# Kernel tuning notes

Measured on AMD Instinct MI355X. Metric: run time of the kernel, lower is better.

The kernel has to match this reference:

```python
import jax, jax.numpy as jnp
import numpy as np

NUM_USERS = 100000
NUM_ITEMS = 50000
D = 64            # args.recdim
N_LAYERS = 3      # args.layer
NNZ = 4800000     # edges in the normalized bipartite adjacency (COO)
N = NUM_USERS + NUM_ITEMS


def setup_inputs() -> dict:
    key = jax.random.key(0)
    k1, k2, k3, k4, k5 = jax.random.split(key, 5)
    # LightGCN inits embeddings with normal(std=0.1)
    user_emb = 0.1 * jax.random.normal(k1, (NUM_USERS, D), dtype=jnp.float32)
    item_emb = 0.1 * jax.random.normal(k2, (NUM_ITEMS, D), dtype=jnp.float32)
    adj_rows = jax.random.randint(k3, (NNZ,), 0, N)
    adj_cols = jax.random.randint(k4, (NNZ,), 0, N)
    # stand-in for D^{-1/2} A D^{-1/2} normalized values
    adj_vals = jax.random.uniform(k5, (NNZ,), dtype=jnp.float32)
    return {"user_emb": user_emb, "item_emb": item_emb,
            "adj_vals": adj_vals, "adj_rows": adj_rows, "adj_cols": adj_cols}


def _spmm(rows, cols, vals, x, n):
    # sparse [n,n] @ dense [n,d] via gather + segment-sum (COO SpMM)
    return jax.ops.segment_sum(vals[:, None] * x[cols], rows, num_segments=n)


def reference(user_emb, item_emb, adj_vals, adj_rows, adj_cols):
    n_users = user_emb.shape[0]
    n = n_users + item_emb.shape[0]
    all_emb = jnp.concatenate([user_emb, item_emb], axis=0)  # [N, D]
    embs = [all_emb]
    for _ in range(N_LAYERS):  # fixed small hop count
        all_emb = _spmm(adj_rows, adj_cols, adj_vals, all_emb, n)
        embs.append(all_emb)
    light_out = jnp.mean(jnp.stack(embs, axis=1), axis=1)  # [N, D]
    users = light_out[:n_users]
    items = light_out[n_users:]
    return users, items
```

## Files before the change

kernel.cpp:

```cpp
#include <hip/hip_runtime.h>


#define NUSERS 100000
#define NITEMS 50000
#define NTOT   150000
#define DIM    64
#define NNZ_E  4800000

#define RPB     256
#define RSH     8
#define NBUCK   586
#define CHUNK_E 8192
#define NPART   ((NNZ_E + CHUNK_E - 1) / CHUNK_E)
#define NCB     37
#define CSH     12
#define NBIN    (RPB * NCB)

__device__ __forceinline__ unsigned short benc(float f) {
    union { float f; unsigned u; } t; t.f = f;
    unsigned r = t.u + 0x7FFFu + ((t.u >> 16) & 1u);
    return (unsigned short)(r >> 16);
}
__device__ __forceinline__ float blo(unsigned g) { return __uint_as_float(g << 16); }
__device__ __forceinline__ float bhi(unsigned g) { return __uint_as_float(g & 0xFFFF0000u); }

__global__ void __launch_bounds__(512)
partA2_kernel(const int* __restrict__ rows, const int* __restrict__ cols,
              const float* __restrict__ vals, int* __restrict__ cntmat,
              int* __restrict__ segoff, int2* __restrict__ tmp) {
    __shared__ int2 buf[CHUNK_E];
    __shared__ int cnt[NBUCK];
    __shared__ int st[512];
    int p = blockIdx.x;
    int c0 = p * CHUNK_E;
    int c1 = c0 + CHUNK_E; if (c1 > NNZ_E) c1 = NNZ_E;
    int nb = c1 - c0;
    int tid = threadIdx.x;
    for (int k = tid; k < NBUCK; k += 512) cnt[k] = 0;
    __syncthreads();
    int rloc[16];
#pragma unroll
    for (int u = 0; u < 16; ++u) {
        int e = c0 + tid + u * 512;
        rloc[u] = (e < c1) ? rows[e] : -1;
        if (rloc[u] >= 0) atomicAdd(&cnt[rloc[u] >> RSH], 1);
    }
    __syncthreads();
    int t0 = tid * 2;
    int cA = (t0     < NBUCK) ? cnt[t0]     : 0;
    int cB = (t0 + 1 < NBUCK) ? cnt[t0 + 1] : 0;
    int s = cA + cB;
    st[tid] = s;
    __syncthreads();
    for (int ofs = 1; ofs < 512; ofs <<= 1) {
        int a = (tid >= ofs) ? st[tid - ofs] : 0;
        __syncthreads();
        st[tid] += a;
        __syncthreads();
    }
    int P = st[tid] - s;
    if (t0 < NBUCK) {
        cnt[t0] = P;
        segoff[(size_t)p * NBUCK + t0] = P;
        cntmat[(size_t)p * NBUCK + t0] = cA;
    }
    if (t0 + 1 < NBUCK) {
        cnt[t0 + 1] = P + cA;
        segoff[(size_t)p * NBUCK + t0 + 1] = P + cA;
        cntmat[(size_t)p * NBUCK + t0 + 1] = cB;
    }
    __syncthreads();
#pragma unroll
    for (int u = 0; u < 16; ++u) {
        int e = c0 + tid + u * 512;
        if (rloc[u] >= 0) {
            int r = rloc[u];
            int b = r >> RSH, rl = r & (RPB - 1);
            int q = atomicAdd(&cnt[b], 1);
            buf[q] = make_int2(cols[e] | (rl << 18), __float_as_int(vals[e]));
        }
    }
    __syncthreads();
    for (int k = tid; k < nb; k += 512)
        tmp[c0 + k] = buf[k];
}

__global__ void __launch_bounds__(1024)
colscan1_kernel(const int* __restrict__ cntmat, int* __restrict__ runoffT,
                int* __restrict__ colTotal) {
    __shared__ int t[1024];
    int b = blockIdx.x;
    int tid = threadIdx.x;
    int v = (tid < NPART) ? cntmat[(size_t)tid * NBUCK + b] : 0;
    t[tid] = v;
    __syncthreads();
    for (int ofs = 1; ofs < 1024; ofs <<= 1) {
        int a = (tid >= ofs) ? t[tid - ofs] : 0;
        __syncthreads();
        t[tid] += a;
        __syncthreads();
    }
    if (tid < NPART) runoffT[(size_t)b * (NPART + 1) + tid] = t[tid] - v;
    if (tid == NPART - 1) {
        runoffT[(size_t)b * (NPART + 1) + NPART] = t[tid];
        colTotal[b] = t[tid];
    }
}

__global__ void __launch_bounds__(1024)
colscan2_kernel(const int* __restrict__ colTotal, int* __restrict__ bptr) {
    __shared__ int t[1024];
    int tid = threadIdx.x;
    int v = (tid < NBUCK) ? colTotal[tid] : 0;
    t[tid] = v;
    __syncthreads();
    for (int ofs = 1; ofs < 1024; ofs <<= 1) {
        int a = (tid >= ofs) ? t[tid - ofs] : 0;
        __syncthreads();
        t[tid] += a;
        __syncthreads();
    }
    if (tid < NBUCK) bptr[tid] = t[tid] - v;
    if (tid == 1023) bptr[NBUCK] = t[1023];
}

__global__ void __launch_bounds__(1024)
partBF_kernel(const int* __restrict__ bptr, const int* __restrict__ runoffT,
              const int* __restrict__ segoff, const int2* __restrict__ tmp,
              unsigned* __restrict__ fin, int* __restrict__ rowptr) {
    __shared__ int cnt[NBIN];
    __shared__ int st[1024];
    __shared__ int runoff[NPART + 1];
    __shared__ int soff[NPART];
    int b = blockIdx.x;
    int bb0 = bptr[b];
    int tid = threadIdx.x;
    for (int k = tid; k < NBIN; k += 1024) cnt[k] = 0;
    if (tid <= NPART) runoff[tid] = runoffT[(size_t)b * (NPART + 1) + tid];
    if (tid < NPART)  soff[tid]   = segoff[(size_t)tid * NBUCK + b];
    __syncthreads();
    int nb = runoff[NPART];
    for (int j = tid; j < nb; j += 1024) {
        int lo = 0, hi = NPART;
        while (hi - lo > 1) { int mid = (lo + hi) >> 1; if (runoff[mid] <= j) lo = mid; else hi = mid; }
        int src = lo * CHUNK_E + soff[lo] + (j - runoff[lo]);
        int x = tmp[src].x;
        int key = ((x >> 18) & 255) * NCB + ((x & 0x3FFFF) >> CSH);
        atomicAdd(&cnt[key], 1);
    }
    __syncthreads();
    int t0 = tid * 10;
    int c[10];
    int s = 0;
#pragma unroll
    for (int u = 0; u < 10; ++u) {
        int idx = t0 + u;
        c[u] = (idx < NBIN) ? cnt[idx] : 0;
        s += c[u];
    }
    st[tid] = s;
    __syncthreads();
    for (int ofs = 1; ofs < 1024; ofs <<= 1) {
        int a = (tid >= ofs) ? st[tid - ofs] : 0;
        __syncthreads();
        st[tid] += a;
        __syncthreads();
    }
    int P = st[tid] - s;
#pragma unroll
    for (int u = 0; u < 10; ++u) {
        int idx = t0 + u;
        if (idx < NBIN) { cnt[idx] = P; P += c[u]; }
    }
    __syncthreads();
    if (tid < RPB) {
        int r = b * RPB + tid;
        if (r < NTOT) rowptr[r] = bb0 + cnt[tid * NCB];
    }
    if (b == NBUCK - 1 && tid == 0) rowptr[NTOT] = bb0 + nb;
    __syncthreads();
    for (int j = tid; j < nb; j += 1024) {
        int lo = 0, hi = NPART;
        while (hi - lo > 1) { int mid = (lo + hi) >> 1; if (runoff[mid] <= j) lo = mid; else hi = mid; }
        int src = lo * CHUNK_E + soff[lo] + (j - runoff[lo]);
        int2 t = tmp[src];
        int x = t.x;
        int key = ((x >> 18) & 255) * NCB + ((x & 0x3FFFF) >> CSH);
        int q = atomicAdd(&cnt[key], 1);
        unsigned qq = (unsigned)__float2int_rn(__int_as_float(t.y) * 4096.f);
        if (qq > 4095u) qq = 4095u;
        fin[bb0 + q] = ((unsigned)x & 0x3FFFFu) | (qq << 20);
    }
}

__global__ void convert_kernel(const float2* __restrict__ user, const float2* __restrict__ item,
                               unsigned* __restrict__ xh2) {
    int i = blockIdx.x * blockDim.x + threadIdx.x;
    if (i >= NTOT * 32) return;
    float2 v = (i < NUSERS * 32) ? user[i] : item[i - NUSERS * 32];
    xh2[i] = (unsigned)benc(v.x) | ((unsigned)benc(v.y) << 16);
}

__global__ void __launch_bounds__(256)
spmm_kernel(const int* __restrict__ rowptr, const unsigned* __restrict__ ed,
            const uint4* __restrict__ xin, uint4* __restrict__ yout,
            const float4* __restrict__ user, const float4* __restrict__ item,
            const uint4* __restrict__ y1, float4* __restrict__ out, int last) {
    int wid = blockIdx.x * (blockDim.x >> 6) + (threadIdx.x >> 6);
    int lane = threadIdx.x & 63;
    int oct = lane >> 3, s = lane & 7;
    int r = wid * 8 + oct;
    if (r >= NTOT) return;
    int start = rowptr[r];
    int end   = rowptr[r + 1];
    const float SCL = 1.f / 4096.f;
    float a0 = 0.f, a1 = 0.f, a2 = 0.f, a3 = 0.f, a4 = 0.f, a5 = 0.f, a6 = 0.f, a7 = 0.f;
    int i = start;
    for (; i + 8 <= end; i += 8) {
        unsigned e[8];
#pragma unroll
        for (int u = 0; u < 8; ++u) e[u] = ed[i + u];
        uint4 g[8];
#pragma unroll
        for (int u = 0; u < 8; ++u) g[u] = xin[(size_t)(e[u] & 0x3FFFFu) * 8 + s];
#pragma unroll
        for (int u = 0; u < 8; ++u) {
            float v = (float)(e[u] >> 20) * SCL;
            a0 += v * blo(g[u].x); a1 += v * bhi(g[u].x);
            a2 += v * blo(g[u].y); a3 += v * bhi(g[u].y);
            a4 += v * blo(g[u].z); a5 += v * bhi(g[u].z);
            a6 += v * blo(g[u].w); a7 += v * bhi(g[u].w);
        }
    }
    for (; i < end; ++i) {
        unsigned e = ed[i];
        uint4 g = xin[(size_t)(e & 0x3FFFFu) * 8 + s];
        float v = (float)(e >> 20) * SCL;
        a0 += v * blo(g.x); a1 += v * bhi(g.x);
        a2 += v * blo(g.y); a3 += v * bhi(g.y);
        a4 += v * blo(g.z); a5 += v * bhi(g.z);
        a6 += v * blo(g.w); a7 += v * bhi(g.w);
    }
    if (!last) {
        uint4 o;
        o.x = (unsigned)benc(a0) | ((unsigned)benc(a1) << 16);
        o.y = (unsigned)benc(a2) | ((unsigned)benc(a3) << 16);
        o.z = (unsigned)benc(a4) | ((unsigned)benc(a5) << 16);
        o.w = (unsigned)benc(a6) | ((unsigned)benc(a7) << 16);
        yout[(size_t)r * 8 + s] = o;
    } else {
        size_t f4 = (size_t)r * 16 + 2 * s;
        float4 x0a = (r < NUSERS) ? user[f4]     : item[f4     - (size_t)NUSERS * 16];
        float4 x0b = (r < NUSERS) ? user[f4 + 1] : item[f4 + 1 - (size_t)NUSERS * 16];
        uint4 u1 = y1[(size_t)r * 8 + s];
        uint4 u2 = xin[(size_t)r * 8 + s];
        float4 oa, ob;
        oa.x = 0.25f * (x0a.x + blo(u1.x) + blo(u2.x) + a0);
        oa.y = 0.25f * (x0a.y + bhi(u1.x) + bhi(u2.x) + a1);
        oa.z = 0.25f * (x0a.z + blo(u1.y) + blo(u2.y) + a2);
        oa.w = 0.25f * (x0a.w + bhi(u1.y) + bhi(u2.y) + a3);
        ob.x = 0.25f * (x0b.x + blo(u1.z) + blo(u2.z) + a4);
        ob.y = 0.25f * (x0b.y + bhi(u1.z) + bhi(u2.z) + a5);
        ob.z = 0.25f * (x0b.z + blo(u1.w) + blo(u2.w) + a6);
        ob.w = 0.25f * (x0b.w + bhi(u1.w) + bhi(u2.w) + a7);
        out[f4]     = oa;
        out[f4 + 1] = ob;
    }
}

extern "C" void kernel_launch(void* const* d_in, const int* in_sizes, int n_in,
                              void* d_out, int out_size, void* d_ws, size_t ws_size,
                              hipStream_t stream) {
    const float* user = (const float*)d_in[0];
    const float* item = (const float*)d_in[1];
    const float* vals = (const float*)d_in[2];
    const int*   rows = (const int*)d_in[3];
    const int*   cols = (const int*)d_in[4];
    float* out = (float*)d_out;

    char* w = (char*)d_ws;
    int2*     tmp      = (int2*)w;     w += (size_t)NNZ_E * 8;
    unsigned* fin      = (unsigned*)w; w += (size_t)NNZ_E * 4;
    unsigned* bufA     = (unsigned*)w; w += (size_t)NTOT * DIM * 2;
    unsigned* bufB     = (unsigned*)w; w += (size_t)NTOT * DIM * 2;
    int*      cntmat   = (int*)w;      w += (size_t)NPART * NBUCK * 4;
    int*      runoffT  = (int*)w;      w += (size_t)NBUCK * (NPART + 1) * 4;
    int*      segoff   = (int*)w;      w += (size_t)NPART * NBUCK * 4;
    int*      rowptr   = (int*)w;      w += (size_t)(NTOT + 1) * 4;
    int*      colTotal = (int*)w;      w += (size_t)NBUCK * 4;
    int*      bptr     = (int*)w;

    const int blk = 256;
    const int gConv = (NTOT * 32 + blk - 1) / blk;
    const int gSpmm = (NTOT / 8 + 3) / 4;

    partA2_kernel<<<NPART, 512, 0, stream>>>(rows, cols, vals, cntmat, segoff, tmp);
    colscan1_kernel<<<NBUCK, 1024, 0, stream>>>(cntmat, runoffT, colTotal);
    colscan2_kernel<<<1, 1024, 0, stream>>>(colTotal, bptr);
    partBF_kernel<<<NBUCK, 1024, 0, stream>>>(bptr, runoffT, segoff, tmp, fin, rowptr);

    convert_kernel<<<gConv, blk, 0, stream>>>((const float2*)user, (const float2*)item, bufA);

    spmm_kernel<<<gSpmm, blk, 0, stream>>>(rowptr, fin, (const uint4*)bufA, (uint4*)bufB,
                                           (const float4*)user, (const float4*)item,
                                           (const uint4*)bufB, (float4*)out, 0);
    spmm_kernel<<<gSpmm, blk, 0, stream>>>(rowptr, fin, (const uint4*)bufB, (uint4*)bufA,
                                           (const float4*)user, (const float4*)item,
                                           (const uint4*)bufB, (float4*)out, 0);
    spmm_kernel<<<gSpmm, blk, 0, stream>>>(rowptr, fin, (const uint4*)bufA, (uint4*)bufA,
                                           (const float4*)user, (const float4*)item,
                                           (const uint4*)bufB, (float4*)out, 1);
}
```

Baseline: 489.3 us.

## Interleave edges of four rows into padded quad groups for vectorized SpMM

```diff
diff --git a/kernel.cpp b/kernel.cpp
--- a/kernel.cpp
+++ b/kernel.cpp
@@ -15,6 +15,8 @@
 #define NCB     37
 #define CSH     12
 #define NBIN    (RPB * NCB)
+#define NOCT    (NBUCK * 64)
+#define FINCAP  6400000
 
 __device__ __forceinline__ unsigned short benc(float f) {
     union { float f; unsigned u; } t; t.f = f;
@@ -86,8 +88,7 @@
 }
 
 __global__ void __launch_bounds__(1024)
-colscan1_kernel(const int* __restrict__ cntmat, int* __restrict__ runoffT,
-                int* __restrict__ colTotal) {
+colscan1_kernel(const int* __restrict__ cntmat, int* __restrict__ runoffT) {
     __shared__ int t[1024];
     int b = blockIdx.x;
     int tid = threadIdx.x;
@@ -101,43 +102,69 @@
         __syncthreads();
     }
     if (tid < NPART) runoffT[(size_t)b * (NPART + 1) + tid] = t[tid] - v;
-    if (tid == NPART - 1) {
-        runoffT[(size_t)b * (NPART + 1) + NPART] = t[tid];
-        colTotal[b] = t[tid];
-    }
+    if (tid == NPART - 1) runoffT[(size_t)b * (NPART + 1) + NPART] = t[tid];
+}
+
+__global__ void __launch_bounds__(256)
+degcnt_kernel(const int* __restrict__ rows, int* __restrict__ deg) {
+    int i = blockIdx.x * 256 + threadIdx.x;
+    int stride = gridDim.x * 256;
+    for (; i < NNZ_E; i += stride) atomicAdd(&deg[rows[i]], 1);
+}
+
+__global__ void __launch_bounds__(256)
+ogmax_kernel(const int* __restrict__ deg, int* __restrict__ p4) {
+    int og = blockIdx.x * 256 + threadIdx.x;
+    if (og >= NOCT) return;
+    int4 d = ((const int4*)deg)[og];
+    int m = max(max(d.x, d.y), max(d.z, d.w));
+    p4[og] = 4 * m;
 }
 
 __global__ void __launch_bounds__(1024)
-colscan2_kernel(const int* __restrict__ colTotal, int* __restrict__ bptr) {
-    __shared__ int t[1024];
+ogscan_kernel(const int* __restrict__ p4, int* __restrict__ ogptr) {
+    __shared__ int st[1024];
     int tid = threadIdx.x;
-    int v = (tid < NBUCK) ? colTotal[tid] : 0;
-    t[tid] = v;
+    int base = tid * 37;
+    int sum = 0;
+#pragma unroll 4
+    for (int u = 0; u < 37; ++u) {
+        int og = base + u;
+        if (og < NOCT) sum += p4[og];
+    }
+    st[tid] = sum;
     __syncthreads();
     for (int ofs = 1; ofs < 1024; ofs <<= 1) {
-        int a = (tid >= ofs) ? t[tid - ofs] : 0;
-        __syncthreads();
-        t[tid] += a;
-        __syncthreads();
-    }
-    if (tid < NBUCK) bptr[tid] = t[tid] - v;
-    if (tid == 1023) bptr[NBUCK] = t[1023];
+        int a = (tid >= ofs) ? st[tid - ofs] : 0;
+        __syncthreads();
+        st[tid] += a;
+        __syncthreads();
+    }
+    int P = st[tid] - sum;
+#pragma unroll 4
+    for (int u = 0; u < 37; ++u) {
+        int og = base + u;
+        if (og < NOCT) { ogptr[og] = P; P += p4[og]; }
+    }
+    if (tid == 1023) ogptr[NOCT] = st[1023];
 }
 
 __global__ void __launch_bounds__(1024)
-partBF_kernel(const int* __restrict__ bptr, const int* __restrict__ runoffT,
-              const int* __restrict__ segoff, const int2* __restrict__ tmp,
-              unsigned* __restrict__ fin, int* __restrict__ rowptr) {
+partBF_kernel(const int* __restrict__ runoffT, const int* __restrict__ segoff,
+              const int2* __restrict__ tmp, const int* __restrict__ ogptr,
+              unsigned* __restrict__ fin) {
     __shared__ int cnt[NBIN];
     __shared__ int st[1024];
     __shared__ int runoff[NPART + 1];
     __shared__ int soff[NPART];
+    __shared__ int rowbase[RPB];
+    __shared__ int ogbase[64];
     int b = blockIdx.x;
-    int bb0 = bptr[b];
     int tid = threadIdx.x;
     for (int k = tid; k < NBIN; k += 1024) cnt[k] = 0;
     if (tid <= NPART) runoff[tid] = runoffT[(size_t)b * (NPART + 1) + tid];
     if (tid < NPART)  soff[tid]   = segoff[(size_t)tid * NBUCK + b];
+    if (tid < 64)     ogbase[tid] = ogptr[b * 64 + tid];
     __syncthreads();
     int nb = runoff[NPART];
     for (int j = tid; j < nb; j += 1024) {
@@ -173,11 +200,7 @@
         if (idx < NBIN) { cnt[idx] = P; P += c[u]; }
     }
     __syncthreads();
-    if (tid < RPB) {
-        int r = b * RPB + tid;
-        if (r < NTOT) rowptr[r] = bb0 + cnt[tid * NCB];
-    }
-    if (b == NBUCK - 1 && tid == 0) rowptr[NTOT] = bb0 + nb;
+    if (tid < RPB) rowbase[tid] = cnt[tid * NCB];
     __syncthreads();
     for (int j = tid; j < nb; j += 1024) {
         int lo = 0, hi = NPART;
@@ -185,11 +208,14 @@
         int src = lo * CHUNK_E + soff[lo] + (j - runoff[lo]);
         int2 t = tmp[src];
         int x = t.x;
-        int key = ((x >> 18) & 255) * NCB + ((x & 0x3FFFF) >> CSH);
+        int rl = (x >> 18) & 255;
+        int key = rl * NCB + ((x & 0x3FFFF) >> CSH);
         int q = atomicAdd(&cnt[key], 1);
+        int i = q - rowbase[rl];
+        int dest = ogbase[rl >> 2] + i * 4 + (rl & 3);
         unsigned qq = (unsigned)__float2int_rn(__int_as_float(t.y) * 4096.f);
         if (qq > 4095u) qq = 4095u;
-        fin[bb0 + q] = ((unsigned)x & 0x3FFFFu) | (qq << 20);
+        fin[dest] = ((unsigned)x & 0x3FFFFu) | (qq << 20);
     }
 }
 
@@ -201,70 +227,97 @@
     xh2[i] = (unsigned)benc(v.x) | ((unsigned)benc(v.y) << 16);
 }
 
-__global__ void __launch_bounds__(256)
-spmm_kernel(const int* __restrict__ rowptr, const unsigned* __restrict__ ed,
-            const uint4* __restrict__ xin, uint4* __restrict__ yout,
-            const float4* __restrict__ user, const float4* __restrict__ item,
-            const uint4* __restrict__ y1, float4* __restrict__ out, int last) {
-    int wid = blockIdx.x * (blockDim.x >> 6) + (threadIdx.x >> 6);
+__global__ void __launch_bounds__(256, 5)
+spmm5_kernel(const int* __restrict__ ogptr, const unsigned* __restrict__ ed,
+             const uint4* __restrict__ xin, uint4* __restrict__ yout,
+             const float4* __restrict__ user, const float4* __restrict__ item,
+             const uint4* __restrict__ y1, float4* __restrict__ out, int last) {
+    int wid  = blockIdx.x * 4 + (threadIdx.x >> 6);
     int lane = threadIdx.x & 63;
-    int oct = lane >> 3, s = lane & 7;
-    int r = wid * 8 + oct;
-    if (r >= NTOT) return;
-    int start = rowptr[r];
-    int end   = rowptr[r + 1];
+    int g    = wid * 8 + (lane >> 3);
+    int s    = lane & 7;
+    int i0   = ogptr[g];
+    int nt   = (ogptr[g + 1] - i0) >> 2;
+    const uint4* eq = (const uint4*)(ed + i0);
     const float SCL = 1.f / 4096.f;
-    float a0 = 0.f, a1 = 0.f, a2 = 0.f, a3 = 0.f, a4 = 0.f, a5 = 0.f, a6 = 0.f, a7 = 0.f;
-    int i = start;
-    for (; i + 8 <= end; i += 8) {
-        unsigned e[8];
-#pragma unroll
-        for (int u = 0; u < 8; ++u) e[u] = ed[i + u];
-        uint4 g[8];
-#pragma unroll
-        for (int u = 0; u < 8; ++u) g[u] = xin[(size_t)(e[u] & 0x3FFFFu) * 8 + s];
-#pragma unroll
-        for (int u = 0; u < 8; ++u) {
-            float v = (float)(e[u] >> 20) * SCL;
-            a0 += v * blo(g[u].x); a1 += v * bhi(g[u].x);
-            a2 += v * blo(g[u].y); a3 += v * bhi(g[u].y);
-            a4 += v * blo(g[u].z); a5 += v * bhi(g[u].z);
-            a6 += v * blo(g[u].w); a7 += v * bhi(g[u].w);
-        }
-    }
-    for (; i < end; ++i) {
-        unsigned e = ed[i];
-        uint4 g = xin[(size_t)(e & 0x3FFFFu) * 8 + s];
-        float v = (float)(e >> 20) * SCL;
-        a0 += v * blo(g.x); a1 += v * bhi(g.x);
-        a2 += v * blo(g.y); a3 += v * bhi(g.y);
-        a4 += v * blo(g.z); a5 += v * bhi(g.z);
-        a6 += v * blo(g.w); a7 += v * bhi(g.w);
-    }
+    float4 A00 = {0,0,0,0}, A01 = {0,0,0,0};
+    float4 A10 = {0,0,0,0}, A11 = {0,0,0,0};
+    float4 A20 = {0,0,0,0}, A21 = {0,0,0,0};
+    float4 A30 = {0,0,0,0}, A31 = {0,0,0,0};
+
+#define ACC(AK0, AK1, E, G) do { \
+        float v = (float)((E) >> 20) * SCL; \
+        AK0.x += v * blo((G).x); AK0.y += v * bhi((G).x); \
+        AK0.z += v * blo((G).y); AK0.w += v * bhi((G).y); \
+        AK1.x += v * blo((G).z); AK1.y += v * bhi((G).z); \
+        AK1.z += v * blo((G).w); AK1.w += v * bhi((G).w); \
+    } while (0)
+
+    int ii = 0;
+    for (; ii + 2 <= nt; ii += 2) {
+        uint4 Ea = eq[ii], Eb = eq[ii + 1];
+        uint4 G0 = xin[(size_t)(Ea.x & 0x3FFFFu) * 8 + s];
+        uint4 G1 = xin[(size_t)(Ea.y & 0x3FFFFu) * 8 + s];
+        uint4 G2 = xin[(size_t)(Ea.z & 0x3FFFFu) * 8 + s];
+        uint4 G3 = xin[(size_t)(Ea.w & 0x3FFFFu) * 8 + s];
+        uint4 G4 = xin[(size_t)(Eb.x & 0x3FFFFu) * 8 + s];
+        uint4 G5 = xin[(size_t)(Eb.y & 0x3FFFFu) * 8 + s];
+        uint4 G6 = xin[(size_t)(Eb.z & 0x3FFFFu) * 8 + s];
+        uint4 G7 = xin[(size_t)(Eb.w & 0x3FFFFu) * 8 + s];
+        ACC(A00, A01, Ea.x, G0); ACC(A10, A11, Ea.y, G1);
+        ACC(A20, A21, Ea.z, G2); ACC(A30, A31, Ea.w, G3);
+        ACC(A00, A01, Eb.x, G4); ACC(A10, A11, Eb.y, G5);
+        ACC(A20, A21, Eb.z, G6); ACC(A30, A31, Eb.w, G7);
+    }
+    if (ii < nt) {
+        uint4 Ea = eq[ii];
+        uint4 G0 = xin[(size_t)(Ea.x & 0x3FFFFu) * 8 + s];
+        uint4 G1 = xin[(size_t)(Ea.y & 0x3FFFFu) * 8 + s];
+        uint4 G2 = xin[(size_t)(Ea.z & 0x3FFFFu) * 8 + s];
+        uint4 G3 = xin[(size_t)(Ea.w & 0x3FFFFu) * 8 + s];
+        ACC(A00, A01, Ea.x, G0); ACC(A10, A11, Ea.y, G1);
+        ACC(A20, A21, Ea.z, G2); ACC(A30, A31, Ea.w, G3);
+    }
+#undef ACC
+
     if (!last) {
-        uint4 o;
-        o.x = (unsigned)benc(a0) | ((unsigned)benc(a1) << 16);
-        o.y = (unsigned)benc(a2) | ((unsigned)benc(a3) << 16);
-        o.z = (unsigned)benc(a4) | ((unsigned)benc(a5) << 16);
-        o.w = (unsigned)benc(a6) | ((unsigned)benc(a7) << 16);
-        yout[(size_t)r * 8 + s] = o;
+#define EPI(K, AK0, AK1) do { \
+        int r = g * 4 + (K); \
+        if (r < NTOT) { \
+            uint4 o; \
+            o.x = (unsigned)benc(AK0.x) | ((unsigned)benc(AK0.y) << 16); \
+            o.y = (unsigned)benc(AK0.z) | ((unsigned)benc(AK0.w) << 16); \
+            o.z = (unsigned)benc(AK1.x) | ((unsigned)benc(AK1.y) << 16); \
+            o.w = (unsigned)benc(AK1.z) | ((unsigned)benc(AK1.w) << 16); \
+            yout[(size_t)r * 8 + s] = o; \
+        } \
+    } while (0)
+        EPI(0, A00, A01); EPI(1, A10, A11); EPI(2, A20, A21); EPI(3, A30, A31);
+#undef EPI
     } else {
-        size_t f4 = (size_t)r * 16 + 2 * s;
-        float4 x0a = (r < NUSERS) ? user[f4]     : item[f4     - (size_t)NUSERS * 16];
-        float4 x0b = (r < NUSERS) ? user[f4 + 1] : item[f4 + 1 - (size_t)NUSERS * 16];
-        uint4 u1 = y1[(size_t)r * 8 + s];
-        uint4 u2 = xin[(size_t)r * 8 + s];
-        float4 oa, ob;
-        oa.x = 0.25f * (x0a.x + blo(u1.x) + blo(u2.x) + a0);
-        oa.y = 0.25f * (x0a.y + bhi(u1.x) + bhi(u2.x) + a1);
-        oa.z = 0.25f * (x0a.z + blo(u1.y) + blo(u2.y) + a2);
-        oa.w = 0.25f * (x0a.w + bhi(u1.y) + bhi(u2.y) + a3);
-        ob.x = 0.25f * (x0b.x + blo(u1.z) + blo(u2.z) + a4);
-        ob.y = 0.25f * (x0b.y + bhi(u1.z) + bhi(u2.z) + a5);
-        ob.z = 0.25f * (x0b.z + blo(u1.w) + blo(u2.w) + a6);
-        ob.w = 0.25f * (x0b.w + bhi(u1.w) + bhi(u2.w) + a7);
-        out[f4]     = oa;
-        out[f4 + 1] = ob;
+#define EPI(K, AK0, AK1) do { \
+        int r = g * 4 + (K); \
+        if (r < NTOT) { \
+            size_t f4 = (size_t)r * 16 + 2 * s; \
+            float4 x0a = (r < NUSERS) ? user[f4]     : item[f4     - (size_t)NUSERS * 16]; \
+            float4 x0b = (r < NUSERS) ? user[f4 + 1] : item[f4 + 1 - (size_t)NUSERS * 16]; \
+            uint4 u1 = y1[(size_t)r * 8 + s]; \
+            uint4 u2 = xin[(size_t)r * 8 + s]; \
+            float4 oa, ob; \
+            oa.x = 0.25f * (x0a.x + blo(u1.x) + blo(u2.x) + AK0.x); \
+            oa.y = 0.25f * (x0a.y + bhi(u1.x) + bhi(u2.x) + AK0.y); \
+            oa.z = 0.25f * (x0a.z + blo(u1.y) + blo(u2.y) + AK0.z); \
+            oa.w = 0.25f * (x0a.w + bhi(u1.y) + bhi(u2.y) + AK0.w); \
+            ob.x = 0.25f * (x0b.x + blo(u1.z) + blo(u2.z) + AK1.x); \
+            ob.y = 0.25f * (x0b.y + bhi(u1.z) + bhi(u2.z) + AK1.y); \
+            ob.z = 0.25f * (x0b.z + blo(u1.w) + blo(u2.w) + AK1.z); \
+            ob.w = 0.25f * (x0b.w + bhi(u1.w) + bhi(u2.w) + AK1.w); \
+            out[f4]     = oa; \
+            out[f4 + 1] = ob; \
+        } \
+    } while (0)
+        EPI(0, A00, A01); EPI(1, A10, A11); EPI(2, A20, A21); EPI(3, A30, A31);
+#undef EPI
     }
 }
 
@@ -279,35 +332,41 @@
     float* out = (float*)d_out;
 
     char* w = (char*)d_ws;
-    int2*     tmp      = (int2*)w;     w += (size_t)NNZ_E * 8;
-    unsigned* fin      = (unsigned*)w; w += (size_t)NNZ_E * 4;
-    unsigned* bufA     = (unsigned*)w; w += (size_t)NTOT * DIM * 2;
-    unsigned* bufB     = (unsigned*)w; w += (size_t)NTOT * DIM * 2;
-    int*      cntmat   = (int*)w;      w += (size_t)NPART * NBUCK * 4;
-    int*      runoffT  = (int*)w;      w += (size_t)NBUCK * (NPART + 1) * 4;
-    int*      segoff   = (int*)w;      w += (size_t)NPART * NBUCK * 4;
-    int*      rowptr   = (int*)w;      w += (size_t)(NTOT + 1) * 4;
-    int*      colTotal = (int*)w;      w += (size_t)NBUCK * 4;
-    int*      bptr     = (int*)w;
+    unsigned* fin     = (unsigned*)w; w += (size_t)FINCAP * 4;
+    int*      cntmat  = (int*)w;      w += (size_t)NPART * NBUCK * 4;
+    int*      runoffT = (int*)w;      w += (size_t)NBUCK * (NPART + 1) * 4;
+    int*      segoff  = (int*)w;      w += (size_t)NPART * NBUCK * 4;
+    int*      deg     = (int*)w;      w += (size_t)(NOCT * 4) * 4;
+    int*      p4      = (int*)w;      w += (size_t)NOCT * 4;
+    int*      ogptr   = (int*)w;      w += (size_t)(NOCT + 1) * 4;
+    char*     X       = w;
+    int2*     tmp     = (int2*)X;
+    unsigned* bufA    = (unsigned*)X;
+    unsigned* bufB    = (unsigned*)(X + (size_t)NTOT * DIM * 2);
 
     const int blk = 256;
     const int gConv = (NTOT * 32 + blk - 1) / blk;
-    const int gSpmm = (NTOT / 8 + 3) / 4;
+    const int gSpmm = NOCT / 32;
+
+    hipMemsetAsync(deg, 0, (size_t)(NOCT * 4) * 4, stream);
+    hipMemsetAsync(fin, 0, (size_t)FINCAP * 4, stream);
 
     partA2_kernel<<<NPART, 512, 0, stream>>>(rows, cols, vals, cntmat, segoff, tmp);
-    colscan1_kernel<<<NBUCK, 1024, 0, stream>>>(cntmat, runoffT, colTotal);
-    colscan2_kernel<<<1, 1024, 0, stream>>>(colTotal, bptr);
-    partBF_kernel<<<NBUCK, 1024, 0, stream>>>(bptr, runoffT, segoff, tmp, fin, rowptr);
+    colscan1_kernel<<<NBUCK, 1024, 0, stream>>>(cntmat, runoffT);
+    degcnt_kernel<<<1024, 256, 0, stream>>>(rows, deg);
+    ogmax_kernel<<<(NOCT + 255) / 256, 256, 0, stream>>>(deg, p4);
+    ogscan_kernel<<<1, 1024, 0, stream>>>(p4, ogptr);
+    partBF_kernel<<<NBUCK, 1024, 0, stream>>>(runoffT, segoff, tmp, ogptr, fin);
 
     convert_kernel<<<gConv, blk, 0, stream>>>((const float2*)user, (const float2*)item, bufA);
 
-    spmm_kernel<<<gSpmm, blk, 0, stream>>>(rowptr, fin, (const uint4*)bufA, (uint4*)bufB,
-                                           (const float4*)user, (const float4*)item,
-                                           (const uint4*)bufB, (float4*)out, 0);
-    spmm_kernel<<<gSpmm, blk, 0, stream>>>(rowptr, fin, (const uint4*)bufB, (uint4*)bufA,
-                                           (const float4*)user, (const float4*)item,
-                                           (const uint4*)bufB, (float4*)out, 0);
-    spmm_kernel<<<gSpmm, blk, 0, stream>>>(rowptr, fin, (const uint4*)bufA, (uint4*)bufA,
-                                           (const float4*)user, (const float4*)item,
-                                           (const uint4*)bufB, (float4*)out, 1);
-}
+    spmm5_kernel<<<gSpmm, blk, 0, stream>>>(ogptr, fin, (const uint4*)bufA, (uint4*)bufB,
+                                            (const float4*)user, (const float4*)item,
+                                            (const uint4*)bufB, (float4*)out, 0);
+    spmm5_kernel<<<gSpmm, blk, 0, stream>>>(ogptr, fin, (const uint4*)bufB, (uint4*)bufA,
+                                            (const float4*)user, (const float4*)item,
+                                            (const uint4*)bufB, (float4*)out, 0);
+    spmm5_kernel<<<gSpmm, blk, 0, stream>>>(ogptr, fin, (const uint4*)bufA, (uint4*)bufA,
+                                            (const float4*)user, (const float4*)item,
+                                            (const uint4*)bufB, (float4*)out, 1);
+}
```

Result: slower. 846.1 us (+72.9%).
